# Kernel optimization log

Measured on AMD Instinct MI355X. Metric: run time of the kernel, lower is better.

## Reference

```python
import jax, jax.numpy as jnp
import numpy as np

N_NODES = 100000
N_EDGES = 3200000
D_IN = 128
D_OUT = 128

def setup_inputs() -> dict:
    key = jax.random.key(0)
    k1, k2, k3, k4, k5 = jax.random.split(key, 5)
    nodes = jnp.arange(N_NODES, dtype=jnp.int64 if jax.config.jax_enable_x64 else jnp.int32)
    features = jax.random.normal(k1, (N_NODES, D_IN), dtype=jnp.float32)
    edge_index = jax.random.randint(k2, (2, N_EDGES), 0, N_NODES)
    # torch nn.Linear(2*D_IN, D_OUT) params, stored as [in, out]
    bound = 1.0 / np.sqrt(2 * D_IN)
    W = jax.random.uniform(k3, (2 * D_IN, D_OUT), minval=-bound, maxval=bound, dtype=jnp.float32)
    b = jax.random.uniform(k4, (D_OUT,), minval=-bound, maxval=bound, dtype=jnp.float32)
    return {"nodes": nodes, "features": features, "edge_index": edge_index, "W": W, "b": b}

def reference(nodes, features, edge_index, W, b):
    # Mean aggregation over full neighbor lists. gcn=False: edges are treated
    # as undirected (neighbors appended for both src and dst), and output is
    # relu(Linear(concat([self_feats, neigh_feats]))).
    N, d = features.shape
    src, dst = edge_index[0], edge_index[1]
    neigh_sum = (jnp.zeros((N, d), features.dtype)
                 .at[src].add(features[dst])
                 .at[dst].add(features[src]))
    cnt = (jnp.zeros((N,), features.dtype)
           .at[src].add(1.0)
           .at[dst].add(1.0))
    neigh_mean = neigh_sum / jnp.maximum(cnt, 1.0)[:, None]
    combined = jnp.concatenate([features[nodes], neigh_mean[nodes]], axis=1)  # [B, 2d]
    return jax.nn.relu(combined @ W + b)
```

## Files before the change

kernel.cpp:

```cpp
#include <hip/hip_runtime.h>
#include <hip/hip_bf16.h>
#include <cmath>

#define D 128
#define MAXNB 1024
#define TEDGE 2048
#define CURPAD 16

typedef __attribute__((ext_vector_type(8))) short bf16x8;
typedef __attribute__((ext_vector_type(4))) float f32x4;
typedef __attribute__((ext_vector_type(2))) float f32x2;

__device__ __forceinline__ unsigned short f2bf(float f) {
    union { __hip_bfloat16 h; unsigned short u; } c;
    c.h = __float2bfloat16(f);
    return c.u;
}

__device__ __forceinline__ void accum8(float* a, uint4 u) {
    a[0] += __uint_as_float(u.x << 16);
    a[1] += __uint_as_float(u.x & 0xffff0000u);
    a[2] += __uint_as_float(u.y << 16);
    a[3] += __uint_as_float(u.y & 0xffff0000u);
    a[4] += __uint_as_float(u.z << 16);
    a[5] += __uint_as_float(u.z & 0xffff0000u);
    a[6] += __uint_as_float(u.w << 16);
    a[7] += __uint_as_float(u.w & 0xffff0000u);
}

__device__ __forceinline__ void accum8f8(float* a, uint2 u) {
    f32x2 p0 = __builtin_amdgcn_cvt_pk_f32_fp8((int)u.x, false);
    f32x2 p1 = __builtin_amdgcn_cvt_pk_f32_fp8((int)u.x, true);
    f32x2 p2 = __builtin_amdgcn_cvt_pk_f32_fp8((int)u.y, false);
    f32x2 p3 = __builtin_amdgcn_cvt_pk_f32_fp8((int)u.y, true);
    a[0] += p0.x; a[1] += p0.y; a[2] += p1.x; a[3] += p1.y;
    a[4] += p2.x; a[5] += p2.y; a[6] += p3.x; a[7] += p3.y;
}

__global__ __launch_bounds__(256) void partition_edges(
    const int* __restrict__ ei, int* __restrict__ cursor,
    int* __restrict__ arena, int pbcap, int E, int nb) {
    __shared__ int cnt[MAXNB];
    __shared__ int off[MAXNB + 1];
    __shared__ int gb[MAXNB];
    __shared__ int sb[256];
    __shared__ int stage[2 * TEDGE];
    __shared__ unsigned short stageb[2 * TEDGE];
    const int t = threadIdx.x;
    const int e0 = blockIdx.x * TEDGE;
    const int eE = min(e0 + TEDGE, E);

#pragma unroll
    for (int k = 0; k < 4; ++k) cnt[t * 4 + k] = 0;
    __syncthreads();

    int s[8], d[8];
    bool v[8];
#pragma unroll
    for (int q = 0; q < 8; ++q) {
        int e = e0 + t + q * 256;
        v[q] = e < eE;
        if (v[q]) { s[q] = ei[e]; d[q] = ei[E + e]; }
    }

#pragma unroll
    for (int q = 0; q < 8; ++q) if (v[q]) {
        atomicAdd(&cnt[s[q] >> 7], 1);
        atomicAdd(&cnt[d[q] >> 7], 1);
    }
    __syncthreads();

    int c0 = cnt[t * 4], c1 = cnt[t * 4 + 1], c2 = cnt[t * 4 + 2], c3 = cnt[t * 4 + 3];
    sb[t] = c0 + c1 + c2 + c3;
    __syncthreads();
    for (int o = 1; o < 256; o <<= 1) {
        int x = (t >= o) ? sb[t - o] : 0;
        __syncthreads();
        sb[t] += x;
        __syncthreads();
    }
    int run = (t > 0) ? sb[t - 1] : 0;
    off[t * 4] = run; run += c0;
    off[t * 4 + 1] = run; run += c1;
    off[t * 4 + 2] = run; run += c2;
    off[t * 4 + 3] = run;
    if (t == 255) off[MAXNB] = sb[255];

    for (int j = t; j < nb; j += 256) {
        int c = cnt[j];
        gb[j] = c ? atomicAdd(&cursor[j * CURPAD], c) : 0;
    }
    __syncthreads();

#pragma unroll
    for (int k = 0; k < 4; ++k) cnt[t * 4 + k] = off[t * 4 + k];
    __syncthreads();

#pragma unroll
    for (int q = 0; q < 8; ++q) if (v[q]) {
        int bs = s[q] >> 7, bd = d[q] >> 7;
        int ps = atomicAdd(&cnt[bs], 1);
        stage[ps] = ((s[q] & 127) << 17) | d[q];
        stageb[ps] = (unsigned short)bs;
        int pd = atomicAdd(&cnt[bd], 1);
        stage[pd] = ((d[q] & 127) << 17) | s[q];
        stageb[pd] = (unsigned short)bd;
    }
    __syncthreads();

    const int total = 2 * (eE - e0);
    for (int p = t; p < total; p += 256) {
        int vv = stage[p];
        int bkt = stageb[p];
        int idx = gb[bkt] + (p - off[bkt]);
        if (idx < pbcap) arena[(size_t)bkt * pbcap + idx] = vv;
    }
}

__global__ __launch_bounds__(256) void bucket_scatter(
    const int* __restrict__ cursor, const int* __restrict__ arena, int pbcap,
    int* __restrict__ deg, int* __restrict__ colp, int cap, int N, int nb) {
    __shared__ int ldeg[128];
    const int t = threadIdx.x;
    for (int b = blockIdx.x; b < nb; b += gridDim.x) {
        if (t < 128) ldeg[t] = 0;
        __syncthreads();
        int cnt = cursor[b * CURPAD];
        if (cnt > pbcap) cnt = pbcap;
        const int* s = arena + (size_t)b * pbcap;
        const size_t cb = (size_t)(b << 7) * cap;
        int i = t;
        for (; i + 768 < cnt; i += 1024) {
            int v0 = s[i], v1 = s[i + 256], v2 = s[i + 512], v3 = s[i + 768];
            int r0 = atomicAdd(&ldeg[v0 >> 17], 1);
            int r1 = atomicAdd(&ldeg[v1 >> 17], 1);
            int r2 = atomicAdd(&ldeg[v2 >> 17], 1);
            int r3 = atomicAdd(&ldeg[v3 >> 17], 1);
            if (r0 < cap) colp[cb + (size_t)(v0 >> 17) * cap + r0] = v0 & 0x1FFFF;
            if (r1 < cap) colp[cb + (size_t)(v1 >> 17) * cap + r1] = v1 & 0x1FFFF;
            if (r2 < cap) colp[cb + (size_t)(v2 >> 17) * cap + r2] = v2 & 0x1FFFF;
            if (r3 < cap) colp[cb + (size_t)(v3 >> 17) * cap + r3] = v3 & 0x1FFFF;
        }
        for (; i < cnt; i += 256) {
            int v = s[i];
            int r = atomicAdd(&ldeg[v >> 17], 1);
            if (r < cap) colp[cb + (size_t)(v >> 17) * cap + r] = v & 0x1FFFF;
        }
        __syncthreads();
        if (t < 128) {
            int node = (b << 7) + t;
            if (node < N) deg[node] = ldeg[t];
        }
        __syncthreads();
    }
}

__global__ __launch_bounds__(256) void bucket_fill(
    const int* __restrict__ ei, int* __restrict__ deg,
    int* __restrict__ colp, int cap, int E) {
    int tid = blockIdx.x * blockDim.x + threadIdx.x;
    int stride = gridDim.x * blockDim.x;
    int e[8], s[8], d[8];
    bool v[8];
#pragma unroll
    for (int q = 0; q < 8; ++q) {
        e[q] = tid + q * stride;
        v[q] = e[q] < E;
    }
#pragma unroll
    for (int q = 0; q < 8; ++q) if (v[q]) { s[q] = ei[e[q]]; d[q] = ei[E + e[q]]; }
    int rs[8], rd[8];
#pragma unroll
    for (int q = 0; q < 8; ++q) if (v[q]) rs[q] = atomicAdd(&deg[s[q]], 1);
#pragma unroll
    for (int q = 0; q < 8; ++q) if (v[q]) rd[q] = atomicAdd(&deg[d[q]], 1);
#pragma unroll
    for (int q = 0; q < 8; ++q) if (v[q] && rs[q] < cap) colp[(size_t)s[q] * cap + rs[q]] = d[q];
#pragma unroll
    for (int q = 0; q < 8; ++q) if (v[q] && rd[q] < cap) colp[(size_t)d[q] * cap + rd[q]] = s[q];
}

__global__ __launch_bounds__(256) void prep_all(
    const float* __restrict__ feat, const float* __restrict__ W,
    int* __restrict__ cursor, uint2* __restrict__ f8,
    unsigned* __restrict__ wb, int n8) {
    const int tid = blockIdx.x * blockDim.x + threadIdx.x;
    const int stride = gridDim.x * blockDim.x;

    for (int i = tid; i < 1024 * CURPAD; i += stride) cursor[i] = 0;

    for (int id = tid; id < 4096; id += stride) {
        int j = id & 127, ks = id >> 7;
        unsigned hi[4], lo[4];
#pragma unroll
        for (int e = 0; e < 4; ++e) {
            float w0 = W[(size_t)(ks * 8 + 2 * e) * 128 + j];
            float w1 = W[(size_t)(ks * 8 + 2 * e + 1) * 128 + j];
            unsigned short h0 = f2bf(w0), h1 = f2bf(w1);
            float l0f = w0 - __uint_as_float((unsigned)h0 << 16);
            float l1f = w1 - __uint_as_float((unsigned)h1 << 16);
            hi[e] = (unsigned)h0 | ((unsigned)h1 << 16);
            lo[e] = (unsigned)f2bf(l0f) | ((unsigned)f2bf(l1f) << 16);
        }
        ((uint4*)wb)[ks * 128 + j] = make_uint4(hi[0], hi[1], hi[2], hi[3]);
        ((uint4*)wb)[4096 + ks * 128 + j] = make_uint4(lo[0], lo[1], lo[2], lo[3]);
    }

    const float4* f = (const float4*)feat;
    for (int i = tid; i < n8; i += stride) {
        float4 a = f[2 * i];
        float4 c = f[2 * i + 1];
        int w0 = __builtin_amdgcn_cvt_pk_fp8_f32(a.x, a.y, 0, false);
        w0 = __builtin_amdgcn_cvt_pk_fp8_f32(a.z, a.w, w0, true);
        int w1 = __builtin_amdgcn_cvt_pk_fp8_f32(c.x, c.y, 0, false);
        w1 = __builtin_amdgcn_cvt_pk_fp8_f32(c.z, c.w, w1, true);
        uint2 r;
        r.x = (unsigned)w0;
        r.y = (unsigned)w1;
        f8[i] = r;
    }
}

__global__ __launch_bounds__(256) void convert_fp8(
    const float4* __restrict__ f, uint2* __restrict__ o, int n8) {
    int i = blockIdx.x * blockDim.x + threadIdx.x;
    int stride = gridDim.x * blockDim.x;
    for (; i < n8; i += stride) {
        float4 a = f[2 * i];
        float4 c = f[2 * i + 1];
        int w0 = __builtin_amdgcn_cvt_pk_fp8_f32(a.x, a.y, 0, false);
        w0 = __builtin_amdgcn_cvt_pk_fp8_f32(a.z, a.w, w0, true);
        int w1 = __builtin_amdgcn_cvt_pk_fp8_f32(c.x, c.y, 0, false);
        w1 = __builtin_amdgcn_cvt_pk_fp8_f32(c.z, c.w, w1, true);
        uint2 r;
        r.x = (unsigned)w0;
        r.y = (unsigned)w1;
        o[i] = r;
    }
}

__global__ __launch_bounds__(256) void convert_bf16(
    const float4* __restrict__ f, uint2* __restrict__ o, int n4) {
    int i = blockIdx.x * blockDim.x + threadIdx.x;
    int stride = gridDim.x * blockDim.x;
    for (; i < n4; i += stride) {
        float4 v = f[i];
        uint2 r;
        r.x = (unsigned)f2bf(v.x) | ((unsigned)f2bf(v.y) << 16);
        r.y = (unsigned)f2bf(v.z) | ((unsigned)f2bf(v.w) << 16);
        o[i] = r;
    }
}

__global__ __launch_bounds__(256) void prepack_w(
    const float* __restrict__ W, unsigned* __restrict__ wb) {
    int id = blockIdx.x * 256 + threadIdx.x;
    if (id >= 4096) return;
    int j = id & 127, ks = id >> 7;
    unsigned hi[4], lo[4];
#pragma unroll
    for (int e = 0; e < 4; ++e) {
        float w0 = W[(size_t)(ks * 8 + 2 * e) * 128 + j];
        float w1 = W[(size_t)(ks * 8 + 2 * e + 1) * 128 + j];
        unsigned short h0 = f2bf(w0), h1 = f2bf(w1);
        float l0f = w0 - __uint_as_float((unsigned)h0 << 16);
        float l1f = w1 - __uint_as_float((unsigned)h1 << 16);
        hi[e] = (unsigned)h0 | ((unsigned)h1 << 16);
        lo[e] = (unsigned)f2bf(l0f) | ((unsigned)f2bf(l1f) << 16);
    }
    ((uint4*)wb)[ks * 128 + j] = make_uint4(hi[0], hi[1], hi[2], hi[3]);
    ((uint4*)wb)[4096 + ks * 128 + j] = make_uint4(lo[0], lo[1], lo[2], lo[3]);
}

__global__ __launch_bounds__(256) void gather_gemm_pad(
    const int* __restrict__ nodes, const float* __restrict__ feat,
    const uint2* __restrict__ fb2,
    const int* __restrict__ deg, const int* __restrict__ colp, int cap,
    const uint4* __restrict__ wb4, const float* __restrict__ b,
    float* __restrict__ out, int B) {
    __shared__ uint4 combQ[512];
    unsigned char* combB = (unsigned char*)combQ;
    const int t = threadIdx.x;
    const int lane = t & 63;
    const int w = t >> 6;
    const int g = lane >> 4;
    const int sub = lane & 15;
    const int base = blockIdx.x * 16;

    {
        int r = t >> 4, sb = t & 15;
        int row = base + r;
        uint4 u = make_uint4(0u, 0u, 0u, 0u);
        if (row < B) {
            const float* fp = feat + (size_t)nodes[row] * D + sb * 8;
            float4 a = *(const float4*)fp;
            float4 c = *(const float4*)(fp + 4);
            u.x = (unsigned)f2bf(a.x) | ((unsigned)f2bf(a.y) << 16);
            u.y = (unsigned)f2bf(a.z) | ((unsigned)f2bf(a.w) << 16);
            u.z = (unsigned)f2bf(c.x) | ((unsigned)f2bf(c.y) << 16);
            u.w = (unsigned)f2bf(c.z) | ((unsigned)f2bf(c.w) << 16);
        }
        int off = (r * 512 + sb * 16) ^ ((r & 7) << 4);
        *(uint4*)(combB + off) = u;
    }

    for (int rq = 0; rq < 4; ++rq) {
        const int rl = w + 4 * rq;
        const int row = base + rl;
        if (row < B) {
            const int node = __builtin_amdgcn_readfirstlane(nodes[row]);
            int degn = deg[node];
            if (degn > cap) degn = cap;
            const int p0 = node * cap;
            float accA[8] = {0, 0, 0, 0, 0, 0, 0, 0};
            float accB[8] = {0, 0, 0, 0, 0, 0, 0, 0};
            int i = 0;
            for (; i + 15 < degn; i += 16) {
                int n0 = colp[p0 + i + g];
                int n1 = colp[p0 + i + 4 + g];
                int n2 = colp[p0 + i + 8 + g];
                int n3 = colp[p0 + i + 12 + g];
                uint2 u0 = fb2[(size_t)n0 * 16 + sub];
                uint2 u1 = fb2[(size_t)n1 * 16 + sub];
                uint2 u2 = fb2[(size_t)n2 * 16 + sub];
                uint2 u3 = fb2[(size_t)n3 * 16 + sub];
                accum8f8(accA, u0);
                accum8f8(accB, u1);
                accum8f8(accA, u2);
                accum8f8(accB, u3);
            }
            for (; i + 7 < degn; i += 8) {
                int n0 = colp[p0 + i + g];
                int n1 = colp[p0 + i + 4 + g];
                uint2 u0 = fb2[(size_t)n0 * 16 + sub];
                uint2 u1 = fb2[(size_t)n1 * 16 + sub];
                accum8f8(accA, u0);
                accum8f8(accB, u1);
            }
            for (; i + 3 < degn; i += 4) {
                int n0 = colp[p0 + i + g];
                accum8f8(accA, fb2[(size_t)n0 * 16 + sub]);
            }
            int rem = degn - i;
            if (g < rem) {
                int n0 = colp[p0 + i + g];
                accum8f8(accB, fb2[(size_t)n0 * 16 + sub]);
            }
            const float inv = (degn > 0) ? 1.0f / (float)degn : 0.0f;
            float vals[8];
#pragma unroll
            for (int k = 0; k < 8; ++k) {
                float v = accA[k] + accB[k];
                v += __shfl_xor(v, 16, 64);
                v += __shfl_xor(v, 32, 64);
                vals[k] = v * inv;
            }
            if (g == 0) {
                unsigned p0u = (unsigned)f2bf(vals[0]) | ((unsigned)f2bf(vals[1]) << 16);
                unsigned p1u = (unsigned)f2bf(vals[2]) | ((unsigned)f2bf(vals[3]) << 16);
                unsigned p2u = (unsigned)f2bf(vals[4]) | ((unsigned)f2bf(vals[5]) << 16);
                unsigned p3u = (unsigned)f2bf(vals[6]) | ((unsigned)f2bf(vals[7]) << 16);
                int off = (rl * 512 + 256 + sub * 16) ^ ((rl & 7) << 4);
                *(uint4*)(combB + off) = make_uint4(p0u, p1u, p2u, p3u);
            }
        } else if (g == 0) {
            int off = (rl * 512 + 256 + sub * 16) ^ ((rl & 7) << 4);
            *(uint4*)(combB + off) = make_uint4(0u, 0u, 0u, 0u);
        }
    }
    __syncthreads();

    const int jl = lane & 15;
    const int kg = lane >> 4;
    const int j0 = w * 32 + jl, j1 = j0 + 16;
    f32x4 acc0 = {0.f, 0.f, 0.f, 0.f};
    f32x4 acc1 = {0.f, 0.f, 0.f, 0.f};
#pragma unroll
    for (int s = 0; s < 8; ++s) {
        int aoff = (jl * 512 + s * 64 + kg * 16) ^ ((jl & 7) << 4);
        bf16x8 a = *(const bf16x8*)(combB + aoff);
        int bi = (s * 4 + kg) * 128;
        bf16x8 bh0 = *(const bf16x8*)&wb4[bi + j0];
        bf16x8 bh1 = *(const bf16x8*)&wb4[bi + j1];
        bf16x8 bl0 = *(const bf16x8*)&wb4[4096 + bi + j0];
        bf16x8 bl1 = *(const bf16x8*)&wb4[4096 + bi + j1];
        acc0 = __builtin_amdgcn_mfma_f32_16x16x32_bf16(a, bh0, acc0, 0, 0, 0);
        acc1 = __builtin_amdgcn_mfma_f32_16x16x32_bf16(a, bh1, acc1, 0, 0, 0);
        acc0 = __builtin_amdgcn_mfma_f32_16x16x32_bf16(a, bl0, acc0, 0, 0, 0);
        acc1 = __builtin_amdgcn_mfma_f32_16x16x32_bf16(a, bl1, acc1, 0, 0, 0);
    }
    const float b0 = b[j0], b1 = b[j1];
    const int r0 = kg * 4;
#pragma unroll
    for (int rg = 0; rg < 4; ++rg) {
        int row = base + r0 + rg;
        if (row < B) {
            out[(size_t)row * D + j0] = fmaxf(acc0[rg] + b0, 0.0f);
            out[(size_t)row * D + j1] = fmaxf(acc1[rg] + b1, 0.0f);
        }
    }
}


__global__ __launch_bounds__(256) void deg_rank(
    const int* __restrict__ ei, int* __restrict__ deg,
    unsigned* __restrict__ rank, int E) {
    int tid = blockIdx.x * blockDim.x + threadIdx.x;
    int stride = gridDim.x * blockDim.x;
    int e[8], s[8], d[8];
    bool v[8];
#pragma unroll
    for (int q = 0; q < 8; ++q) {
        e[q] = tid + q * stride;
        v[q] = e[q] < E;
    }
#pragma unroll
    for (int q = 0; q < 8; ++q) if (v[q]) { s[q] = ei[e[q]]; d[q] = ei[E + e[q]]; }
    int rs[8], rd[8];
#pragma unroll
    for (int q = 0; q < 8; ++q) if (v[q]) rs[q] = atomicAdd(&deg[s[q]], 1);
#pragma unroll
    for (int q = 0; q < 8; ++q) if (v[q]) rd[q] = atomicAdd(&deg[d[q]], 1);
#pragma unroll
    for (int q = 0; q < 8; ++q)
        if (v[q]) rank[e[q]] = (unsigned)rs[q] | ((unsigned)rd[q] << 16);
}

__global__ __launch_bounds__(256) void scan_block(
    const int* __restrict__ deg, int* __restrict__ rowptr,
    int* __restrict__ bsum, int N) {
    __shared__ int lds[256];
    const int t = threadIdx.x;
    const int base = blockIdx.x * 1024 + t * 4;
    int v[4];
#pragma unroll
    for (int k = 0; k < 4; ++k) v[k] = (base + k < N) ? deg[base + k] : 0;
    lds[t] = v[0] + v[1] + v[2] + v[3];
    __syncthreads();
    for (int off = 1; off < 256; off <<= 1) {
        int x = (t >= off) ? lds[t - off] : 0;
        __syncthreads();
        lds[t] += x;
        __syncthreads();
    }
    if (t == 255) bsum[blockIdx.x] = lds[255];
    int run = (t > 0) ? lds[t - 1] : 0;
#pragma unroll
    for (int k = 0; k < 4; ++k) {
        if (base + k < N) rowptr[base + k] = run;
        run += v[k];
    }
}

__global__ __launch_bounds__(1024) void scan_aux(int* __restrict__ bsum, int nb) {
    __shared__ int lds[1024];
    const int t = threadIdx.x;
    int v = (t < nb) ? bsum[t] : 0;
    lds[t] = v;
    __syncthreads();
    for (int off = 1; off < 1024; off <<= 1) {
        int x = (t >= off) ? lds[t - off] : 0;
        __syncthreads();
        lds[t] += x;
        __syncthreads();
    }
    if (t < nb) bsum[t] = lds[t] - v;
}

__global__ __launch_bounds__(256) void scan_finalize(
    int* __restrict__ rowptr, const int* __restrict__ bsum, int N, int twoE) {
    int i = blockIdx.x * blockDim.x + threadIdx.x;
    if (i == 0) rowptr[N] = twoE;
    if (i >= N) return;
    rowptr[i] += bsum[i >> 10];
}

__global__ __launch_bounds__(256) void csr_fill2(
    const int* __restrict__ ei, const int* __restrict__ rowptr,
    const unsigned* __restrict__ rank, int* __restrict__ col, int E) {
    int tid = blockIdx.x * blockDim.x + threadIdx.x;
    int stride = gridDim.x * blockDim.x;
    int e[8], s[8], d[8], ps[8], pd[8];
    unsigned r[8];
    bool v[8];
#pragma unroll
    for (int q = 0; q < 8; ++q) {
        e[q] = tid + q * stride;
        v[q] = e[q] < E;
    }
#pragma unroll
    for (int q = 0; q < 8; ++q) if (v[q]) { s[q] = ei[e[q]]; d[q] = ei[E + e[q]]; r[q] = rank[e[q]]; }
#pragma unroll
    for (int q = 0; q < 8; ++q) if (v[q]) { ps[q] = rowptr[s[q]]; pd[q] = rowptr[d[q]]; }
#pragma unroll
    for (int q = 0; q < 8; ++q) if (v[q]) {
        col[ps[q] + (int)(r[q] & 0xffffu)] = d[q];
        col[pd[q] + (int)(r[q] >> 16)] = s[q];
    }
}

__global__ __launch_bounds__(256) void gather_gemm(
    const int* __restrict__ nodes, const uint4* __restrict__ fb4,
    const int* __restrict__ rowptr, const int* __restrict__ col,
    const float* __restrict__ W, const float* __restrict__ b,
    float* __restrict__ out, int B) {
    __shared__ float comb[16][256];
    const int t = threadIdx.x;
    const int lane = t & 63;
    const int w = t >> 6;
    const int g = lane >> 4;
    const int sub = lane & 15;
    const int base = blockIdx.x * 16;
    {
        int r = t >> 4, sb = t & 15;
        int row = base + r;
        float a[8] = {0, 0, 0, 0, 0, 0, 0, 0};
        if (row < B) accum8(a, fb4[(size_t)nodes[row] * 16 + sb]);
        *(float4*)&comb[r][sb * 8] = make_float4(a[0], a[1], a[2], a[3]);
        *(float4*)&comb[r][sb * 8 + 4] = make_float4(a[4], a[5], a[6], a[7]);
    }
    for (int rq = 0; rq < 4; ++rq) {
        const int rl = w + 4 * rq;
        const int row = base + rl;
        if (row < B) {
            const int node = __builtin_amdgcn_readfirstlane(nodes[row]);
            const int p0 = rowptr[node], p1 = rowptr[node + 1];
            float accA[8] = {0, 0, 0, 0, 0, 0, 0, 0};
            float accB[8] = {0, 0, 0, 0, 0, 0, 0, 0};
            int i = p0;
            for (; i + 7 < p1; i += 8) {
                int na = col[i + g];
                int nb = col[i + 4 + g];
                uint4 ua = fb4[(size_t)na * 16 + sub];
                uint4 ub = fb4[(size_t)nb * 16 + sub];
                accum8(accA, ua);
                accum8(accB, ub);
            }
            for (; i + 3 < p1; i += 4) {
                int na = col[i + g];
                accum8(accA, fb4[(size_t)na * 16 + sub]);
            }
            int rem = p1 - i;
            if (g < rem) {
                int na = col[i + g];
                accum8(accB, fb4[(size_t)na * 16 + sub]);
            }
            const int degn = p1 - p0;
            const float inv = (degn > 0) ? 1.0f / (float)degn : 0.0f;
            float vals[8];
#pragma unroll
            for (int k = 0; k < 8; ++k) {
                float v = accA[k] + accB[k];
                v += __shfl_xor(v, 16, 64);
                v += __shfl_xor(v, 32, 64);
                vals[k] = v * inv;
            }
            if (g == 0) {
                *(float4*)&comb[rl][128 + sub * 8] =
                    make_float4(vals[0], vals[1], vals[2], vals[3]);
                *(float4*)&comb[rl][128 + sub * 8 + 4] =
                    make_float4(vals[4], vals[5], vals[6], vals[7]);
            }
        } else if (g == 0) {
            float4 z = make_float4(0.f, 0.f, 0.f, 0.f);
            *(float4*)&comb[rl][128 + sub * 8] = z;
            *(float4*)&comb[rl][128 + sub * 8 + 4] = z;
        }
    }
    __syncthreads();
    const int j = t & 127;
    const int rr = t >> 7;
    float acc[8];
    const float bj = b[j];
#pragma unroll
    for (int r = 0; r < 8; ++r) acc[r] = bj;
    for (int k4 = 0; k4 < 64; ++k4) {
        float w0 = W[(size_t)(4 * k4 + 0) * 128 + j];
        float w1 = W[(size_t)(4 * k4 + 1) * 128 + j];
        float w2 = W[(size_t)(4 * k4 + 2) * 128 + j];
        float w3 = W[(size_t)(4 * k4 + 3) * 128 + j];
#pragma unroll
        for (int r = 0; r < 8; ++r) {
            float4 c = *(const float4*)&comb[2 * r + rr][4 * k4];
            acc[r] = fmaf(c.x, w0, acc[r]);
            acc[r] = fmaf(c.y, w1, acc[r]);
            acc[r] = fmaf(c.z, w2, acc[r]);
            acc[r] = fmaf(c.w, w3, acc[r]);
        }
    }
#pragma unroll
    for (int r = 0; r < 8; ++r) {
        int row = base + 2 * r + rr;
        if (row < B) out[(size_t)row * D + j] = fmaxf(acc[r], 0.0f);
    }
}

__global__ __launch_bounds__(256) void edge_scatter(
    const int* __restrict__ ei, const float* __restrict__ feat,
    float* __restrict__ nsum, float* __restrict__ cnt, int E) {
    long long tid = (long long)blockIdx.x * blockDim.x + threadIdx.x;
    int e = (int)(tid >> 7);
    if (e >= E) return;
    int d = (int)(tid & 127);
    int src = ei[e];
    int dst = ei[E + e];
    atomicAdd(&nsum[(size_t)src * D + d], feat[(size_t)dst * D + d]);
    atomicAdd(&nsum[(size_t)dst * D + d], feat[(size_t)src * D + d]);
    if (d == 0) {
        atomicAdd(&cnt[src], 1.0f);
        atomicAdd(&cnt[dst], 1.0f);
    }
}

__global__ __launch_bounds__(256) void sage_out(
    const int* __restrict__ nodes, const float* __restrict__ feat,
    const float* nsum, const float* __restrict__ cnt,
    const float* __restrict__ W, const float* __restrict__ b,
    float* out, int B) {
    __shared__ float comb[16][256];
    const int t = threadIdx.x;
    const int j = t & 127;
    const int rr = t >> 7;
    const int base = blockIdx.x * 16;
    for (int r = 0; r < 16; ++r) {
        int row = base + r;
        float v = 0.0f;
        if (row < B) {
            int node = nodes[row];
            if (t < 128) v = feat[(size_t)node * D + t];
            else v = nsum[(size_t)node * D + (t - 128)] / fmaxf(cnt[node], 1.0f);
        }
        comb[r][t] = v;
    }
    __syncthreads();
    float acc[8];
    const float bj = b[j];
#pragma unroll
    for (int r = 0; r < 8; ++r) acc[r] = bj;
#pragma unroll 4
    for (int k = 0; k < 256; ++k) {
        float wj = W[(size_t)k * 128 + j];
#pragma unroll
        for (int r = 0; r < 8; ++r) acc[r] += comb[rr + 2 * r][k] * wj;
    }
#pragma unroll
    for (int r = 0; r < 8; ++r) {
        int row = base + rr + 2 * r;
        if (row < B) out[(size_t)row * D + j] = fmaxf(acc[r], 0.0f);
    }
}

extern "C" void kernel_launch(void* const* d_in, const int* in_sizes, int n_in,
                              void* d_out, int out_size, void* d_ws, size_t ws_size,
                              hipStream_t stream) {
    const int* nodes = (const int*)d_in[0];
    const float* feat = (const float*)d_in[1];
    const int* ei = (const int*)d_in[2];
    const float* W = (const float*)d_in[3];
    const float* b = (const float*)d_in[4];
    float* out = (float*)d_out;

    const int B = in_sizes[0];
    const int N = in_sizes[1] / D;
    const int E = in_sizes[2] / 2;
    const int twoE = 2 * E;
    const int nscan = (N + 1023) / 1024;
    const int n4 = N * (D / 4);
    const int n8 = N * (D / 8);
    const size_t ws_ints = ws_size / sizeof(int);

    const int nb = (N + 127) >> 7;
    double avgpb = nb > 0 ? (2.0 * (double)E) / (double)nb : 0.0;
    int pbcap = (int)(avgpb + 8.0 * sqrt(avgpb > 0.0 ? avgpb : 0.0) + 64.0);
    pbcap = (pbcap + 3) & ~3;
    const size_t u_arena = (size_t)nb * pbcap;
    const size_t u_fp8 = (size_t)N * 32;
    const size_t u0 = (u_arena > u_fp8) ? u_arena : u_fp8;
    const size_t o0_deg = (u0 + 3) & ~(size_t)3;
    const size_t o0_cur = (o0_deg + N + 3) & ~(size_t)3;
    const size_t o0_wb = o0_cur + 1024 * CURPAD;
    const size_t o0_colp = o0_wb + 32768;
    long long cap0_ll = (ws_ints > o0_colp) ? (long long)((ws_ints - o0_colp) / N) : 0;
    int cap0 = (cap0_ll > 192) ? 192 : (int)cap0_ll;

    const size_t o1_deg = (size_t)N * 32;
    const size_t o1_wb = (o1_deg + N + 3) & ~(size_t)3;
    const size_t o1_colp = o1_wb + 32768;
    long long cap_ll = (ws_ints > o1_colp) ? (long long)((ws_ints - o1_colp) / N) : 0;
    int cap = (cap_ll > 192) ? 192 : (int)cap_ll;

    const size_t o_deg = 0;
    const size_t o_rowptr = (o_deg + N + 3) & ~(size_t)3;
    const size_t o_bsum = (o_rowptr + N + 1 + 3) & ~(size_t)3;
    const size_t o_col = (o_bsum + 1024 + 3) & ~(size_t)3;
    const size_t o_rank = (o_col + twoE + 3) & ~(size_t)3;
    const size_t tail = ((size_t)E > (size_t)N * 64) ? (size_t)E : (size_t)N * 64;
    const size_t need2 = (o_rank + tail) * sizeof(int);

    if (cap0 >= 128 && N <= (1 << 17) && nb <= MAXNB && E > 0) {
        int* wsI = (int*)d_ws;
        int* arena = wsI;
        unsigned* f8 = (unsigned*)wsI;
        int* deg = wsI + o0_deg;
        int* cursor = wsI + o0_cur;
        unsigned* wbp = (unsigned*)(wsI + o0_wb);
        int* colp = wsI + o0_colp;

        prep_all<<<64, 256, 0, stream>>>(feat, W, cursor, (uint2*)f8, wbp, 0);

        int pblocks = (E + TEDGE - 1) / TEDGE;
        partition_edges<<<pblocks, 256, 0, stream>>>(ei, cursor, arena, pbcap, E, nb);

        bucket_scatter<<<nb, 256, 0, stream>>>(
            cursor, arena, pbcap, deg, colp, cap0, N, nb);

        convert_fp8<<<(n8 + 1023) / 1024, 256, 0, stream>>>(
            (const float4*)feat, (uint2*)f8, n8);

        gather_gemm_pad<<<(B + 15) / 16, 256, 0, stream>>>(
            nodes, feat, (const uint2*)f8, deg, colp, cap0,
            (const uint4*)wbp, b, out, B);
    } else if (cap >= 128) {
        int* wsI = (int*)d_ws;
        unsigned* f8 = (unsigned*)wsI;
        int* deg = wsI + o1_deg;
        unsigned* wbp = (unsigned*)(wsI + o1_wb);
        int* colp = wsI + o1_colp;

        hipMemsetAsync(deg, 0, (size_t)N * sizeof(int), stream);

        prepack_w<<<16, 256, 0, stream>>>(W, wbp);

        convert_fp8<<<(n8 + 1023) / 1024, 256, 0, stream>>>(
            (const float4*)feat, (uint2*)f8, n8);

        int eb8 = (E + 2047) / 2048;
        bucket_fill<<<eb8, 256, 0, stream>>>(ei, deg, colp, cap, E);

        gather_gemm_pad<<<(B + 15) / 16, 256, 0, stream>>>(
            nodes, feat, (const uint2*)f8, deg, colp, cap,
            (const uint4*)wbp, b, out, B);
    } else if (ws_size >= need2 && nscan <= 1024) {
        int* wsI = (int*)d_ws;
        int* deg = wsI + o_deg;
        int* rowptr = wsI + o_rowptr;
        int* bsum = wsI + o_bsum;
        int* col = wsI + o_col;
        unsigned* rank = (unsigned*)(wsI + o_rank);
        unsigned* fbu = (unsigned*)(wsI + o_rank);

        hipMemsetAsync(deg, 0, (size_t)N * sizeof(int), stream);

        int eb8 = (E + 2047) / 2048;
        deg_rank<<<eb8, 256, 0, stream>>>(ei, deg, rank, E);
        scan_block<<<nscan, 256, 0, stream>>>(deg, rowptr, bsum, N);
        scan_aux<<<1, 1024, 0, stream>>>(bsum, nscan);
        scan_finalize<<<(N + 255) / 256, 256, 0, stream>>>(rowptr, bsum, N, twoE);
        csr_fill2<<<eb8, 256, 0, stream>>>(ei, rowptr, rank, col, E);
        convert_bf16<<<(n4 + 1023) / 1024, 256, 0, stream>>>(
            (const float4*)feat, (uint2*)fbu, n4);
        gather_gemm<<<(B + 15) / 16, 256, 0, stream>>>(
            nodes, (const uint4*)fbu, rowptr, col, W, b, out, B);
    } else {
        float* nsum = out;
        float* cnt = (float*)d_ws;
        hipMemsetAsync(d_out, 0, (size_t)N * D * sizeof(float), stream);
        hipMemsetAsync(d_ws, 0, (size_t)N * sizeof(float), stream);
        long long tot = (long long)E * 128;
        int blocks = (int)((tot + 255) / 256);
        edge_scatter<<<blocks, 256, 0, stream>>>(ei, feat, nsum, cnt, E);
        sage_out<<<(B + 15) / 16, 256, 0, stream>>>(nodes, feat, nsum, cnt, W, b, out, B);
    }
}
```

Before: 385.5 us.

## Widen edge buckets to 256 nodes, binary-search bucket ids, prefetch neighbor indices

Edge buckets now cover 256 nodes instead of 128, so there are half as many. partition_edges takes 4096 edges per block and drops the per-entry bucket-id staging array; it recovers each entry's bucket with a binary search over the offset table instead. bucket_scatter runs with 512 threads. The gather loop software-prefetches the next batch of column indices and accumulates in packed float2 vectors, aiming to hide index-load latency and cut instruction count. The costs are higher register pressure, more LDS use per partition block, and roughly ten extra LDS reads per element for the binary search.

Result: no change. 381.1 us (-1.1%).

```diff
diff --git a/kernel.cpp b/kernel.cpp
--- a/kernel.cpp
+++ b/kernel.cpp
@@ -4,7 +4,9 @@
 
 #define D 128
 #define MAXNB 1024
-#define TEDGE 2048
+#define TEDGE 4096
+#define BSH 8
+#define BNODES 256
 #define CURPAD 16
 
 typedef __attribute__((ext_vector_type(8))) short bf16x8;
@@ -28,13 +30,11 @@
     a[7] += __uint_as_float(u.w & 0xffff0000u);
 }
 
-__device__ __forceinline__ void accum8f8(float* a, uint2 u) {
-    f32x2 p0 = __builtin_amdgcn_cvt_pk_f32_fp8((int)u.x, false);
-    f32x2 p1 = __builtin_amdgcn_cvt_pk_f32_fp8((int)u.x, true);
-    f32x2 p2 = __builtin_amdgcn_cvt_pk_f32_fp8((int)u.y, false);
-    f32x2 p3 = __builtin_amdgcn_cvt_pk_f32_fp8((int)u.y, true);
-    a[0] += p0.x; a[1] += p0.y; a[2] += p1.x; a[3] += p1.y;
-    a[4] += p2.x; a[5] += p2.y; a[6] += p3.x; a[7] += p3.y;
+__device__ __forceinline__ void accum8f8v(f32x2* a, uint2 u) {
+    a[0] += __builtin_amdgcn_cvt_pk_f32_fp8((int)u.x, false);
+    a[1] += __builtin_amdgcn_cvt_pk_f32_fp8((int)u.x, true);
+    a[2] += __builtin_amdgcn_cvt_pk_f32_fp8((int)u.y, false);
+    a[3] += __builtin_amdgcn_cvt_pk_f32_fp8((int)u.y, true);
 }
 
 __global__ __launch_bounds__(256) void partition_edges(
@@ -45,7 +45,6 @@
     __shared__ int gb[MAXNB];
     __shared__ int sb[256];
     __shared__ int stage[2 * TEDGE];
-    __shared__ unsigned short stageb[2 * TEDGE];
     const int t = threadIdx.x;
     const int e0 = blockIdx.x * TEDGE;
     const int eE = min(e0 + TEDGE, E);
@@ -54,19 +53,19 @@
     for (int k = 0; k < 4; ++k) cnt[t * 4 + k] = 0;
     __syncthreads();
 
-    int s[8], d[8];
-    bool v[8];
-#pragma unroll
-    for (int q = 0; q < 8; ++q) {
+    int s[16], d[16];
+    bool v[16];
+#pragma unroll
+    for (int q = 0; q < 16; ++q) {
         int e = e0 + t + q * 256;
         v[q] = e < eE;
         if (v[q]) { s[q] = ei[e]; d[q] = ei[E + e]; }
     }
 
 #pragma unroll
-    for (int q = 0; q < 8; ++q) if (v[q]) {
-        atomicAdd(&cnt[s[q] >> 7], 1);
-        atomicAdd(&cnt[d[q] >> 7], 1);
+    for (int q = 0; q < 16; ++q) if (v[q]) {
+        atomicAdd(&cnt[s[q] >> BSH], 1);
+        atomicAdd(&cnt[d[q] >> BSH], 1);
     }
     __syncthreads();
 
@@ -97,41 +96,42 @@
     __syncthreads();
 
 #pragma unroll
-    for (int q = 0; q < 8; ++q) if (v[q]) {
-        int bs = s[q] >> 7, bd = d[q] >> 7;
-        int ps = atomicAdd(&cnt[bs], 1);
-        stage[ps] = ((s[q] & 127) << 17) | d[q];
-        stageb[ps] = (unsigned short)bs;
-        int pd = atomicAdd(&cnt[bd], 1);
-        stage[pd] = ((d[q] & 127) << 17) | s[q];
-        stageb[pd] = (unsigned short)bd;
+    for (int q = 0; q < 16; ++q) if (v[q]) {
+        int ps = atomicAdd(&cnt[s[q] >> BSH], 1);
+        stage[ps] = ((s[q] & (BNODES - 1)) << 17) | d[q];
+        int pd = atomicAdd(&cnt[d[q] >> BSH], 1);
+        stage[pd] = ((d[q] & (BNODES - 1)) << 17) | s[q];
     }
     __syncthreads();
 
     const int total = 2 * (eE - e0);
     for (int p = t; p < total; p += 256) {
         int vv = stage[p];
-        int bkt = stageb[p];
-        int idx = gb[bkt] + (p - off[bkt]);
-        if (idx < pbcap) arena[(size_t)bkt * pbcap + idx] = vv;
-    }
-}
-
-__global__ __launch_bounds__(256) void bucket_scatter(
+        int lo = 0, hi = MAXNB;
+        while (hi - lo > 1) {
+            int mid = (lo + hi) >> 1;
+            if (off[mid] <= p) lo = mid; else hi = mid;
+        }
+        int idx = gb[lo] + (p - off[lo]);
+        if (idx < pbcap) arena[(size_t)lo * pbcap + idx] = vv;
+    }
+}
+
+__global__ __launch_bounds__(512) void bucket_scatter(
     const int* __restrict__ cursor, const int* __restrict__ arena, int pbcap,
     int* __restrict__ deg, int* __restrict__ colp, int cap, int N, int nb) {
-    __shared__ int ldeg[128];
+    __shared__ int ldeg[BNODES];
     const int t = threadIdx.x;
     for (int b = blockIdx.x; b < nb; b += gridDim.x) {
-        if (t < 128) ldeg[t] = 0;
+        if (t < BNODES) ldeg[t] = 0;
         __syncthreads();
         int cnt = cursor[b * CURPAD];
         if (cnt > pbcap) cnt = pbcap;
         const int* s = arena + (size_t)b * pbcap;
-        const size_t cb = (size_t)(b << 7) * cap;
+        const size_t cb = ((size_t)b << BSH) * cap;
         int i = t;
-        for (; i + 768 < cnt; i += 1024) {
-            int v0 = s[i], v1 = s[i + 256], v2 = s[i + 512], v3 = s[i + 768];
+        for (; i + 1536 < cnt; i += 2048) {
+            int v0 = s[i], v1 = s[i + 512], v2 = s[i + 1024], v3 = s[i + 1536];
             int r0 = atomicAdd(&ldeg[v0 >> 17], 1);
             int r1 = atomicAdd(&ldeg[v1 >> 17], 1);
             int r2 = atomicAdd(&ldeg[v2 >> 17], 1);
@@ -141,14 +141,14 @@
             if (r2 < cap) colp[cb + (size_t)(v2 >> 17) * cap + r2] = v2 & 0x1FFFF;
             if (r3 < cap) colp[cb + (size_t)(v3 >> 17) * cap + r3] = v3 & 0x1FFFF;
         }
-        for (; i < cnt; i += 256) {
+        for (; i < cnt; i += 512) {
             int v = s[i];
             int r = atomicAdd(&ldeg[v >> 17], 1);
             if (r < cap) colp[cb + (size_t)(v >> 17) * cap + r] = v & 0x1FFFF;
         }
         __syncthreads();
-        if (t < 128) {
-            int node = (b << 7) + t;
+        if (t < BNODES) {
+            int node = (b << BSH) + t;
             if (node < N) deg[node] = ldeg[t];
         }
         __syncthreads();
@@ -312,48 +312,62 @@
             int degn = deg[node];
             if (degn > cap) degn = cap;
             const int p0 = node * cap;
-            float accA[8] = {0, 0, 0, 0, 0, 0, 0, 0};
-            float accB[8] = {0, 0, 0, 0, 0, 0, 0, 0};
+            f32x2 accA[4] = {{0.f, 0.f}, {0.f, 0.f}, {0.f, 0.f}, {0.f, 0.f}};
+            f32x2 accB[4] = {{0.f, 0.f}, {0.f, 0.f}, {0.f, 0.f}, {0.f, 0.f}};
             int i = 0;
+            int nn0 = 0, nn1 = 0, nn2 = 0, nn3 = 0;
+            if (degn >= 16) {
+                nn0 = colp[p0 + g];
+                nn1 = colp[p0 + 4 + g];
+                nn2 = colp[p0 + 8 + g];
+                nn3 = colp[p0 + 12 + g];
+            }
             for (; i + 15 < degn; i += 16) {
-                int n0 = colp[p0 + i + g];
-                int n1 = colp[p0 + i + 4 + g];
-                int n2 = colp[p0 + i + 8 + g];
-                int n3 = colp[p0 + i + 12 + g];
+                int n0 = nn0, n1 = nn1, n2 = nn2, n3 = nn3;
+                if (i + 31 < degn) {
+                    nn0 = colp[p0 + i + 16 + g];
+                    nn1 = colp[p0 + i + 20 + g];
+                    nn2 = colp[p0 + i + 24 + g];
+                    nn3 = colp[p0 + i + 28 + g];
+                }
                 uint2 u0 = fb2[(size_t)n0 * 16 + sub];
                 uint2 u1 = fb2[(size_t)n1 * 16 + sub];
                 uint2 u2 = fb2[(size_t)n2 * 16 + sub];
                 uint2 u3 = fb2[(size_t)n3 * 16 + sub];
-                accum8f8(accA, u0);
-                accum8f8(accB, u1);
-                accum8f8(accA, u2);
-                accum8f8(accB, u3);
+                accum8f8v(accA, u0);
+                accum8f8v(accB, u1);
+                accum8f8v(accA, u2);
+                accum8f8v(accB, u3);
             }
             for (; i + 7 < degn; i += 8) {
                 int n0 = colp[p0 + i + g];
                 int n1 = colp[p0 + i + 4 + g];
                 uint2 u0 = fb2[(size_t)n0 * 16 + sub];
                 uint2 u1 = fb2[(size_t)n1 * 16 + sub];
-                accum8f8(accA, u0);
-                accum8f8(accB, u1);
+                accum8f8v(accA, u0);
+                accum8f8v(accB, u1);
             }
             for (; i + 3 < degn; i += 4) {
                 int n0 = colp[p0 + i + g];
-                accum8f8(accA, fb2[(size_t)n0 * 16 + sub]);
+                accum8f8v(accA, fb2[(size_t)n0 * 16 + sub]);
             }
             int rem = degn - i;
             if (g < rem) {
                 int n0 = colp[p0 + i + g];
-                accum8f8(accB, fb2[(size_t)n0 * 16 + sub]);
+                accum8f8v(accB, fb2[(size_t)n0 * 16 + sub]);
             }
             const float inv = (degn > 0) ? 1.0f / (float)degn : 0.0f;
             float vals[8];
 #pragma unroll
-            for (int k = 0; k < 8; ++k) {
-                float v = accA[k] + accB[k];
-                v += __shfl_xor(v, 16, 64);
-                v += __shfl_xor(v, 32, 64);
-                vals[k] = v * inv;
+            for (int k = 0; k < 4; ++k) {
+                f32x2 v2 = accA[k] + accB[k];
+                float vx = v2.x, vy = v2.y;
+                vx += __shfl_xor(vx, 16, 64);
+                vx += __shfl_xor(vx, 32, 64);
+                vy += __shfl_xor(vy, 16, 64);
+                vy += __shfl_xor(vy, 32, 64);
+                vals[2 * k] = vx * inv;
+                vals[2 * k + 1] = vy * inv;
             }
             if (g == 0) {
                 unsigned p0u = (unsigned)f2bf(vals[0]) | ((unsigned)f2bf(vals[1]) << 16);
@@ -669,7 +683,7 @@
     const int n8 = N * (D / 8);
     const size_t ws_ints = ws_size / sizeof(int);
 
-    const int nb = (N + 127) >> 7;
+    const int nb = (N + BNODES - 1) >> BSH;
     double avgpb = nb > 0 ? (2.0 * (double)E) / (double)nb : 0.0;
     int pbcap = (int)(avgpb + 8.0 * sqrt(avgpb > 0.0 ? avgpb : 0.0) + 64.0);
     pbcap = (pbcap + 3) & ~3;
@@ -711,7 +725,7 @@
         int pblocks = (E + TEDGE - 1) / TEDGE;
         partition_edges<<<pblocks, 256, 0, stream>>>(ei, cursor, arena, pbcap, E, nb);
 
-        bucket_scatter<<<nb, 256, 0, stream>>>(
+        bucket_scatter<<<nb, 512, 0, stream>>>(
             cursor, arena, pbcap, deg, colp, cap0, N, nb);
 
         convert_fp8<<<(n8 + 1023) / 1024, 256, 0, stream>>>(
```

## Use 256-node buckets, larger edge tiles, and binary-search bucket lookup

Applied to the files above, without the earlier changes.

Bucket width in the edge partition grows from 128 to 256 nodes and each partition block now handles 4096 edges instead of 2048. The per-entry bucket id array in shared memory is removed; the write-out phase instead finds each entry's bucket with a binary search over the offset table. bucket_scatter now runs 512 threads per block to match the larger buckets. The intent is fewer, larger contiguous arena runs and fewer blocks and cursor atomics. The cost is more per-thread binary-search work, more registers for 16 edges per thread, and a larger shared-memory stage that may reduce occupancy.

Measured after the change: 379.6 us. No clear change (-1.5%).

```diff
diff --git a/kernel.cpp b/kernel.cpp
--- a/kernel.cpp
+++ b/kernel.cpp
@@ -4,7 +4,9 @@
 
 #define D 128
 #define MAXNB 1024
-#define TEDGE 2048
+#define TEDGE 4096
+#define BSH 8
+#define BNODES 256
 #define CURPAD 16
 
 typedef __attribute__((ext_vector_type(8))) short bf16x8;
@@ -45,7 +47,6 @@
     __shared__ int gb[MAXNB];
     __shared__ int sb[256];
     __shared__ int stage[2 * TEDGE];
-    __shared__ unsigned short stageb[2 * TEDGE];
     const int t = threadIdx.x;
     const int e0 = blockIdx.x * TEDGE;
     const int eE = min(e0 + TEDGE, E);
@@ -54,19 +55,19 @@
     for (int k = 0; k < 4; ++k) cnt[t * 4 + k] = 0;
     __syncthreads();
 
-    int s[8], d[8];
-    bool v[8];
-#pragma unroll
-    for (int q = 0; q < 8; ++q) {
+    int s[16], d[16];
+    bool v[16];
+#pragma unroll
+    for (int q = 0; q < 16; ++q) {
         int e = e0 + t + q * 256;
         v[q] = e < eE;
         if (v[q]) { s[q] = ei[e]; d[q] = ei[E + e]; }
     }
 
 #pragma unroll
-    for (int q = 0; q < 8; ++q) if (v[q]) {
-        atomicAdd(&cnt[s[q] >> 7], 1);
-        atomicAdd(&cnt[d[q] >> 7], 1);
+    for (int q = 0; q < 16; ++q) if (v[q]) {
+        atomicAdd(&cnt[s[q] >> BSH], 1);
+        atomicAdd(&cnt[d[q] >> BSH], 1);
     }
     __syncthreads();
 
@@ -97,41 +98,42 @@
     __syncthreads();
 
 #pragma unroll
-    for (int q = 0; q < 8; ++q) if (v[q]) {
-        int bs = s[q] >> 7, bd = d[q] >> 7;
-        int ps = atomicAdd(&cnt[bs], 1);
-        stage[ps] = ((s[q] & 127) << 17) | d[q];
-        stageb[ps] = (unsigned short)bs;
-        int pd = atomicAdd(&cnt[bd], 1);
-        stage[pd] = ((d[q] & 127) << 17) | s[q];
-        stageb[pd] = (unsigned short)bd;
+    for (int q = 0; q < 16; ++q) if (v[q]) {
+        int ps = atomicAdd(&cnt[s[q] >> BSH], 1);
+        stage[ps] = ((s[q] & (BNODES - 1)) << 17) | d[q];
+        int pd = atomicAdd(&cnt[d[q] >> BSH], 1);
+        stage[pd] = ((d[q] & (BNODES - 1)) << 17) | s[q];
     }
     __syncthreads();
 
     const int total = 2 * (eE - e0);
     for (int p = t; p < total; p += 256) {
         int vv = stage[p];
-        int bkt = stageb[p];
-        int idx = gb[bkt] + (p - off[bkt]);
-        if (idx < pbcap) arena[(size_t)bkt * pbcap + idx] = vv;
-    }
-}
-
-__global__ __launch_bounds__(256) void bucket_scatter(
+        int lo = 0, hi = MAXNB;
+        while (hi - lo > 1) {
+            int mid = (lo + hi) >> 1;
+            if (off[mid] <= p) lo = mid; else hi = mid;
+        }
+        int idx = gb[lo] + (p - off[lo]);
+        if (idx < pbcap) arena[(size_t)lo * pbcap + idx] = vv;
+    }
+}
+
+__global__ __launch_bounds__(512) void bucket_scatter(
     const int* __restrict__ cursor, const int* __restrict__ arena, int pbcap,
     int* __restrict__ deg, int* __restrict__ colp, int cap, int N, int nb) {
-    __shared__ int ldeg[128];
+    __shared__ int ldeg[BNODES];
     const int t = threadIdx.x;
     for (int b = blockIdx.x; b < nb; b += gridDim.x) {
-        if (t < 128) ldeg[t] = 0;
+        if (t < BNODES) ldeg[t] = 0;
         __syncthreads();
         int cnt = cursor[b * CURPAD];
         if (cnt > pbcap) cnt = pbcap;
         const int* s = arena + (size_t)b * pbcap;
-        const size_t cb = (size_t)(b << 7) * cap;
+        const size_t cb = ((size_t)b << BSH) * cap;
         int i = t;
-        for (; i + 768 < cnt; i += 1024) {
-            int v0 = s[i], v1 = s[i + 256], v2 = s[i + 512], v3 = s[i + 768];
+        for (; i + 1536 < cnt; i += 2048) {
+            int v0 = s[i], v1 = s[i + 512], v2 = s[i + 1024], v3 = s[i + 1536];
             int r0 = atomicAdd(&ldeg[v0 >> 17], 1);
             int r1 = atomicAdd(&ldeg[v1 >> 17], 1);
             int r2 = atomicAdd(&ldeg[v2 >> 17], 1);
@@ -141,14 +143,14 @@
             if (r2 < cap) colp[cb + (size_t)(v2 >> 17) * cap + r2] = v2 & 0x1FFFF;
             if (r3 < cap) colp[cb + (size_t)(v3 >> 17) * cap + r3] = v3 & 0x1FFFF;
         }
-        for (; i < cnt; i += 256) {
+        for (; i < cnt; i += 512) {
             int v = s[i];
             int r = atomicAdd(&ldeg[v >> 17], 1);
             if (r < cap) colp[cb + (size_t)(v >> 17) * cap + r] = v & 0x1FFFF;
         }
         __syncthreads();
-        if (t < 128) {
-            int node = (b << 7) + t;
+        if (t < BNODES) {
+            int node = (b << BSH) + t;
             if (node < N) deg[node] = ldeg[t];
         }
         __syncthreads();
@@ -669,12 +671,13 @@
     const int n8 = N * (D / 8);
     const size_t ws_ints = ws_size / sizeof(int);
 
-    const int nb = (N + 127) >> 7;
+    const int nb = (N + BNODES - 1) >> BSH;
     double avgpb = nb > 0 ? (2.0 * (double)E) / (double)nb : 0.0;
     int pbcap = (int)(avgpb + 8.0 * sqrt(avgpb > 0.0 ? avgpb : 0.0) + 64.0);
     pbcap = (pbcap + 3) & ~3;
     const size_t u_arena = (size_t)nb * pbcap;
     const size_t u_fp8 = (size_t)N * 32;
+
     const size_t u0 = (u_arena > u_fp8) ? u_arena : u_fp8;
     const size_t o0_deg = (u0 + 3) & ~(size_t)3;
     const size_t o0_cur = (o0_deg + N + 3) & ~(size_t)3;
@@ -697,7 +700,9 @@
     const size_t tail = ((size_t)E > (size_t)N * 64) ? (size_t)E : (size_t)N * 64;
     const size_t need2 = (o_rank + tail) * sizeof(int);
 
-    if (cap0 >= 128 && N <= (1 << 17) && nb <= MAXNB && E > 0) {
+    const bool t0ok = (N <= (1 << 17)) && (nb <= MAXNB) && (E > 0);
+
+    if (cap0 >= 128 && t0ok) {
         int* wsI = (int*)d_ws;
         int* arena = wsI;
         unsigned* f8 = (unsigned*)wsI;
@@ -711,7 +716,7 @@
         int pblocks = (E + TEDGE - 1) / TEDGE;
         partition_edges<<<pblocks, 256, 0, stream>>>(ei, cursor, arena, pbcap, E, nb);
 
-        bucket_scatter<<<nb, 256, 0, stream>>>(
+        bucket_scatter<<<nb, 512, 0, stream>>>(
             cursor, arena, pbcap, deg, colp, cap0, N, nb);
 
         convert_fp8<<<(n8 + 1023) / 1024, 256, 0, stream>>>(
```
